# Performance work log

Measured on AMD Instinct MI355X. Metric: run time of the kernel, lower is better.

The kernel has to match this reference:

```python
import jax, jax.numpy as jnp
import numpy as np

NUM_JOINTS = 24
NUM_GRAPHS = 65536
# SMPL-like humanoid kinematic tree: parent[i] < i, root has parent -1
PARENT_TREE = np.array([-1, 0, 1, 2, 3, 0, 5, 6, 7, 0, 9, 10, 11, 12, 11,
                        14, 15, 16, 11, 18, 19, 20, 12, 22], dtype=np.int64)


def rotation_6d_to_matrix(d6):
    # standard 6D rotation representation -> 3x3 rotation matrix (rows b1,b2,b3)
    a1, a2 = d6[..., :3], d6[..., 3:]
    b1 = a1 / (jnp.linalg.norm(a1, axis=-1, keepdims=True) + 1e-12)
    a2p = a2 - jnp.sum(b1 * a2, axis=-1, keepdims=True) * b1
    b2 = a2p / (jnp.linalg.norm(a2p, axis=-1, keepdims=True) + 1e-12)
    b3 = jnp.cross(b1, b2)
    return jnp.stack([b1, b2, b3], axis=-2)  # [..., 3, 3]


def setup_inputs() -> dict:
    key = jax.random.key(0)
    k1, k2 = jax.random.split(key)
    B, N = NUM_GRAPHS, NUM_JOINTS
    x = jax.random.normal(k1, (B * N, 6), dtype=jnp.float32)
    offset = jax.random.normal(k2, (B * N, 3), dtype=jnp.float32)
    parent = jnp.tile(jnp.asarray(PARENT_TREE), B)  # [B*N], valid tree per graph
    return {"x": x, "parent": parent, "offset": offset, "num_graphs": B}


def reference(x, parent, offset, num_graphs):
    B = num_graphs
    x = x.reshape(B, -1, x.shape[-1])            # [B, N, 6]
    N = x.shape[1]
    offset = offset.reshape(B, N, 3)             # [B, N, 3]
    parent_np = np.asarray(parent).reshape(B, -1)[0]  # static tree structure

    T = rotation_6d_to_matrix(x)                 # [B, N, 3, 3] local rotations

    pos = [None] * N   # world positions per joint, each [B, 3]
    rot = [None] * N   # world rotations per joint, each [B, 3, 3]
    for i in range(N):  # N is small/static; parent-before-child order
        p = int(parent_np[i])
        if p == -1:
            pos[i] = jnp.zeros((B, 3), dtype=x.dtype)
            rot[i] = T[:, i]
        else:
            pos[i] = jnp.einsum('bij,bj->bi', rot[p], offset[:, i]) + pos[p]
            rot[i] = jnp.einsum('bij,bjk->bik', rot[p], T[:, i])

    positions = jnp.stack(pos, axis=1)           # [B, N, 3]
    return positions.reshape(-1, 3)              # [B*N, 3]
```

## Files before the change

### kernel.cpp

```cpp
#include <hip/hip_runtime.h>
#include <math.h>


#define GPB 128
#define PAD 129

__device__ __forceinline__ void rot6d(float a0, float a1, float a2,
                                      float a3, float a4, float a5,
                                      float T[9]) {
    float n1 = sqrtf(a0*a0 + a1*a1 + a2*a2) + 1e-12f;
    float i1 = 1.0f / n1;
    float b1x = a0*i1, b1y = a1*i1, b1z = a2*i1;
    float d = b1x*a3 + b1y*a4 + b1z*a5;
    float ax = a3 - d*b1x, ay = a4 - d*b1y, az = a5 - d*b1z;
    float n2 = sqrtf(ax*ax + ay*ay + az*az) + 1e-12f;
    float i2 = 1.0f / n2;
    float b2x = ax*i2, b2y = ay*i2, b2z = az*i2;
    T[0] = b1x; T[1] = b1y; T[2] = b1z;
    T[3] = b2x; T[4] = b2y; T[5] = b2z;
    T[6] = b1y*b2z - b1z*b2y;
    T[7] = b1z*b2x - b1x*b2z;
    T[8] = b1x*b2y - b1y*b2x;
}

__device__ __forceinline__ void load_x(const float4* __restrict__ x4, long base4,
                                       int c, int t, float4 xr[9]) {
#pragma unroll
    for (int k = 0; k < 9; ++k) {
        int i = k * GPB + t;
        int g = i / 9, e = i - g * 9;
        xr[k] = x4[base4 + (long)g * 36 + c * 9 + e];
    }
}

__device__ __forceinline__ void load_o(const float2* __restrict__ o2, long base2,
                                       int c, int t, float2 orr[9]) {
#pragma unroll
    for (int k = 0; k < 9; ++k) {
        int i = k * GPB + t;
        int g = i / 9, e = i - g * 9;
        orr[k] = o2[base2 + (long)g * 36 + c * 9 + e];
    }
}

__device__ __forceinline__ void write_lds(float* xs, float* os_, int t,
                                          const float4 xr[9], const float2 orr[9]) {
#pragma unroll
    for (int k = 0; k < 9; ++k) {
        int i = k * GPB + t;
        int g = i / 9, e = i - g * 9;
        xs[(4*e+0)*PAD + g] = xr[k].x;
        xs[(4*e+1)*PAD + g] = xr[k].y;
        xs[(4*e+2)*PAD + g] = xr[k].z;
        xs[(4*e+3)*PAD + g] = xr[k].w;
        os_[(2*e+0)*PAD + g] = orr[k].x;
        os_[(2*e+1)*PAD + g] = orr[k].y;
    }
}

template<int J>
__device__ __forceinline__ void joint_step(const float* xs, const float* os_,
                                           float* outs, int t,
                                           float R[9], float Pc[3]) {
    constexpr int jl = J % 6;
    float a0 = xs[(jl*6+0)*PAD + t];
    float a1 = xs[(jl*6+1)*PAD + t];
    float a2 = xs[(jl*6+2)*PAD + t];
    float a3 = xs[(jl*6+3)*PAD + t];
    float a4 = xs[(jl*6+4)*PAD + t];
    float a5 = xs[(jl*6+5)*PAD + t];
    float T[9];
    rot6d(a0, a1, a2, a3, a4, a5, T);
    float o0 = os_[(jl*3+0)*PAD + t];
    float o1 = os_[(jl*3+1)*PAD + t];
    float o2 = os_[(jl*3+2)*PAD + t];
    float p0 = R[0]*o0 + R[1]*o1 + R[2]*o2 + Pc[0];
    float p1 = R[3]*o0 + R[4]*o1 + R[5]*o2 + Pc[1];
    float p2 = R[6]*o0 + R[7]*o1 + R[8]*o2 + Pc[2];
    float Rn[9];
#pragma unroll
    for (int i = 0; i < 3; ++i)
#pragma unroll
        for (int k = 0; k < 3; ++k)
            Rn[i*3+k] = R[i*3+0]*T[0+k] + R[i*3+1]*T[3+k] + R[i*3+2]*T[6+k];
#pragma unroll
    for (int i = 0; i < 9; ++i) R[i] = Rn[i];
    Pc[0] = p0; Pc[1] = p1; Pc[2] = p2;
    outs[(J*3+0)*PAD + t] = p0;
    outs[(J*3+1)*PAD + t] = p1;
    outs[(J*3+2)*PAD + t] = p2;
}

__global__ __launch_bounds__(GPB) void fk_kernel(const float* __restrict__ x,
                                                 const float* __restrict__ off,
                                                 float* __restrict__ out, int B) {
    __shared__ float xs[36 * PAD];
    __shared__ float os_[18 * PAD];
    __shared__ float outs[72 * PAD];
    int t = threadIdx.x;
    long gb0 = (long)blockIdx.x * GPB;
    const float4* x4 = (const float4*)x;
    const float2* o2g = (const float2*)off;
    long xb4 = gb0 * 36;
    long ob2 = gb0 * 36;

    float4 xr[9]; float2 orr[9];
    float R[9], Pc[3], R0[9], R11[9], P11[3], R12[9], P12[3];

    load_x(x4, xb4, 0, t, xr);
    load_o(o2g, ob2, 0, t, orr);
    write_lds(xs, os_, t, xr, orr);
    __syncthreads();

    load_x(x4, xb4, 1, t, xr);
    load_o(o2g, ob2, 1, t, orr);
    {
        float a0 = xs[0*PAD+t], a1 = xs[1*PAD+t], a2 = xs[2*PAD+t];
        float a3 = xs[3*PAD+t], a4 = xs[4*PAD+t], a5 = xs[5*PAD+t];
        rot6d(a0, a1, a2, a3, a4, a5, R);
        Pc[0] = Pc[1] = Pc[2] = 0.0f;
        outs[0*PAD+t] = 0.0f; outs[1*PAD+t] = 0.0f; outs[2*PAD+t] = 0.0f;
#pragma unroll
        for (int i = 0; i < 9; ++i) R0[i] = R[i];
    }
    joint_step<1>(xs, os_, outs, t, R, Pc);
    joint_step<2>(xs, os_, outs, t, R, Pc);
    joint_step<3>(xs, os_, outs, t, R, Pc);
    joint_step<4>(xs, os_, outs, t, R, Pc);
#pragma unroll
    for (int i = 0; i < 9; ++i) R[i] = R0[i];
    Pc[0] = Pc[1] = Pc[2] = 0.0f;
    joint_step<5>(xs, os_, outs, t, R, Pc);
    __syncthreads();
    write_lds(xs, os_, t, xr, orr);
    __syncthreads();

    load_x(x4, xb4, 2, t, xr);
    load_o(o2g, ob2, 2, t, orr);
    joint_step<6>(xs, os_, outs, t, R, Pc);
    joint_step<7>(xs, os_, outs, t, R, Pc);
    joint_step<8>(xs, os_, outs, t, R, Pc);
#pragma unroll
    for (int i = 0; i < 9; ++i) R[i] = R0[i];
    Pc[0] = Pc[1] = Pc[2] = 0.0f;
    joint_step<9>(xs, os_, outs, t, R, Pc);
    joint_step<10>(xs, os_, outs, t, R, Pc);
    joint_step<11>(xs, os_, outs, t, R, Pc);
#pragma unroll
    for (int i = 0; i < 9; ++i) R11[i] = R[i];
    P11[0] = Pc[0]; P11[1] = Pc[1]; P11[2] = Pc[2];
    __syncthreads();
    write_lds(xs, os_, t, xr, orr);
    __syncthreads();

    load_x(x4, xb4, 3, t, xr);
    load_o(o2g, ob2, 3, t, orr);
    joint_step<12>(xs, os_, outs, t, R, Pc);
#pragma unroll
    for (int i = 0; i < 9; ++i) R12[i] = R[i];
    P12[0] = Pc[0]; P12[1] = Pc[1]; P12[2] = Pc[2];
    joint_step<13>(xs, os_, outs, t, R, Pc);
#pragma unroll
    for (int i = 0; i < 9; ++i) R[i] = R11[i];
    Pc[0] = P11[0]; Pc[1] = P11[1]; Pc[2] = P11[2];
    joint_step<14>(xs, os_, outs, t, R, Pc);
    joint_step<15>(xs, os_, outs, t, R, Pc);
    joint_step<16>(xs, os_, outs, t, R, Pc);
    joint_step<17>(xs, os_, outs, t, R, Pc);
    __syncthreads();
    write_lds(xs, os_, t, xr, orr);
    __syncthreads();

#pragma unroll
    for (int i = 0; i < 9; ++i) R[i] = R11[i];
    Pc[0] = P11[0]; Pc[1] = P11[1]; Pc[2] = P11[2];
    joint_step<18>(xs, os_, outs, t, R, Pc);
    joint_step<19>(xs, os_, outs, t, R, Pc);
    joint_step<20>(xs, os_, outs, t, R, Pc);
    joint_step<21>(xs, os_, outs, t, R, Pc);
#pragma unroll
    for (int i = 0; i < 9; ++i) R[i] = R12[i];
    Pc[0] = P12[0]; Pc[1] = P12[1]; Pc[2] = P12[2];
    joint_step<22>(xs, os_, outs, t, R, Pc);
    joint_step<23>(xs, os_, outs, t, R, Pc);
    __syncthreads();

    float4* out4 = (float4*)out;
    long outb4 = gb0 * 18;
#pragma unroll
    for (int k = 0; k < 18; ++k) {
        int i = k * GPB + t;
        int g = i / 18, e = i - g * 18;
        float4 v;
        v.x = outs[(4*e+0)*PAD + g];
        v.y = outs[(4*e+1)*PAD + g];
        v.z = outs[(4*e+2)*PAD + g];
        v.w = outs[(4*e+3)*PAD + g];
        out4[outb4 + i] = v;
    }
}

__global__ __launch_bounds__(256) void fk_tail(const float* __restrict__ x,
                                               const float* __restrict__ off,
                                               float* __restrict__ out,
                                               int b0, int B) {
    int b = b0 + blockIdx.x * blockDim.x + threadIdx.x;
    if (b >= B) return;
    const float* xb = x + (size_t)b * 144;
    const float* ob = off + (size_t)b * 72;
    float* P = out + (size_t)b * 72;
    float R[9], Pc[3], R0[9], R11[9], P11[3], R12[9], P12[3];
    {
        rot6d(xb[0], xb[1], xb[2], xb[3], xb[4], xb[5], R);
        Pc[0] = Pc[1] = Pc[2] = 0.0f;
        P[0] = P[1] = P[2] = 0.0f;
        for (int i = 0; i < 9; ++i) R0[i] = R[i];
    }
    const int parent[24] = {-1,0,1,2,3,0,5,6,7,0,9,10,11,12,11,14,15,16,11,18,19,20,12,22};
    for (int j = 1; j < 24; ++j) {
        int p = parent[j];
        float Rp[9], Pp[3];
        if (p == 0)       { for (int i=0;i<9;++i) Rp[i]=R0[i];  Pp[0]=Pp[1]=Pp[2]=0.f; }
        else if (j==14||j==18) { for (int i=0;i<9;++i) Rp[i]=R11[i]; Pp[0]=P11[0];Pp[1]=P11[1];Pp[2]=P11[2]; }
        else if (j==22)   { for (int i=0;i<9;++i) Rp[i]=R12[i]; Pp[0]=P12[0];Pp[1]=P12[1];Pp[2]=P12[2]; }
        else              { for (int i=0;i<9;++i) Rp[i]=R[i];   Pp[0]=Pc[0];Pp[1]=Pc[1];Pp[2]=Pc[2]; }
        float T[9];
        rot6d(xb[j*6+0],xb[j*6+1],xb[j*6+2],xb[j*6+3],xb[j*6+4],xb[j*6+5],T);
        float o0=ob[j*3+0],o1=ob[j*3+1],o2=ob[j*3+2];
        Pc[0]=Rp[0]*o0+Rp[1]*o1+Rp[2]*o2+Pp[0];
        Pc[1]=Rp[3]*o0+Rp[4]*o1+Rp[5]*o2+Pp[1];
        Pc[2]=Rp[6]*o0+Rp[7]*o1+Rp[8]*o2+Pp[2];
        for (int i=0;i<3;++i) for (int k=0;k<3;++k) {
            float s=0.f; for (int m=0;m<3;++m) s+=Rp[i*3+m]*T[m*3+k];
            R[i*3+k]=s;
        }
        P[j*3+0]=Pc[0]; P[j*3+1]=Pc[1]; P[j*3+2]=Pc[2];
        if (j==11) { for (int i=0;i<9;++i) R11[i]=R[i]; P11[0]=Pc[0];P11[1]=Pc[1];P11[2]=Pc[2]; }
        if (j==12) { for (int i=0;i<9;++i) R12[i]=R[i]; P12[0]=Pc[0];P12[1]=Pc[1];P12[2]=Pc[2]; }
    }
}

extern "C" void kernel_launch(void* const* d_in, const int* in_sizes, int n_in,
                              void* d_out, int out_size, void* d_ws, size_t ws_size,
                              hipStream_t stream) {
    const float* x   = (const float*)d_in[0];
    const float* off = (const float*)d_in[2];
    float* out = (float*)d_out;
    int B = in_sizes[0] / 144;
    int nb = B / GPB;
    if (nb > 0)
        fk_kernel<<<nb, GPB, 0, stream>>>(x, off, out, B);
    int rem = B - nb * GPB;
    if (rem > 0)
        fk_tail<<<(rem + 255) / 256, 256, 0, stream>>>(x, off, out, nb * GPB, B);
}
```

Baseline: 22.08 us.

## Prefetch all input chunks up front, halve block size, flush outputs early

Loads all four joint chunks of x and offset into registers at kernel start instead of software-pipelining one chunk ahead, halves graphs per block to 64 so the register arrays fit, and writes the first half of the output positions to global memory mid-kernel. The aim is more memory-level parallelism per thread and overlap of output stores with later compute. Holding 54 vector registers of input per thread sharply raises register pressure and may cut occupancy despite the smaller blocks. Launch bounds now hint one block per CU minimum. The tail kernel also hardcodes the root-child test.

```diff
diff --git a/kernel.cpp b/kernel.cpp
--- a/kernel.cpp
+++ b/kernel.cpp
@@ -2,8 +2,8 @@
 #include <math.h>
 
 
-#define GPB 128
-#define PAD 129
+#define GPB 64
+#define PAD 65
 
 __device__ __forceinline__ void rot6d(float a0, float a1, float a2,
                                       float a3, float a4, float a5,
@@ -21,26 +21,6 @@
     T[6] = b1y*b2z - b1z*b2y;
     T[7] = b1z*b2x - b1x*b2z;
     T[8] = b1x*b2y - b1y*b2x;
-}
-
-__device__ __forceinline__ void load_x(const float4* __restrict__ x4, long base4,
-                                       int c, int t, float4 xr[9]) {
-#pragma unroll
-    for (int k = 0; k < 9; ++k) {
-        int i = k * GPB + t;
-        int g = i / 9, e = i - g * 9;
-        xr[k] = x4[base4 + (long)g * 36 + c * 9 + e];
-    }
-}
-
-__device__ __forceinline__ void load_o(const float2* __restrict__ o2, long base2,
-                                       int c, int t, float2 orr[9]) {
-#pragma unroll
-    for (int k = 0; k < 9; ++k) {
-        int i = k * GPB + t;
-        int g = i / 9, e = i - g * 9;
-        orr[k] = o2[base2 + (long)g * 36 + c * 9 + e];
-    }
 }
 
 __device__ __forceinline__ void write_lds(float* xs, float* os_, int t,
@@ -91,9 +71,25 @@
     outs[(J*3+2)*PAD + t] = p2;
 }
 
-__global__ __launch_bounds__(GPB) void fk_kernel(const float* __restrict__ x,
-                                                 const float* __restrict__ off,
-                                                 float* __restrict__ out, int B) {
+template<int H>
+__device__ __forceinline__ void flush_half(const float* outs, float4* out4,
+                                           long outb4, int t) {
+#pragma unroll
+    for (int k = 0; k < 9; ++k) {
+        int i = k * GPB + t;
+        int g = i / 9, e = i - g * 9;
+        float4 v;
+        v.x = outs[(36*H + 4*e + 0)*PAD + g];
+        v.y = outs[(36*H + 4*e + 1)*PAD + g];
+        v.z = outs[(36*H + 4*e + 2)*PAD + g];
+        v.w = outs[(36*H + 4*e + 3)*PAD + g];
+        out4[outb4 + (long)g*18 + 9*H + e] = v;
+    }
+}
+
+__global__ __launch_bounds__(GPB, 1) void fk_kernel(const float* __restrict__ x,
+                                                    const float* __restrict__ off,
+                                                    float* __restrict__ out, int B) {
     __shared__ float xs[36 * PAD];
     __shared__ float os_[18 * PAD];
     __shared__ float outs[72 * PAD];
@@ -104,16 +100,30 @@
     long xb4 = gb0 * 36;
     long ob2 = gb0 * 36;
 
-    float4 xr[9]; float2 orr[9];
+    float4 xr[4][9];
+    float2 orr[4][9];
+#pragma unroll
+    for (int c = 0; c < 4; ++c) {
+#pragma unroll
+        for (int k = 0; k < 9; ++k) {
+            int i = k * GPB + t;
+            int g = i / 9, e = i - g * 9;
+            xr[c][k] = x4[xb4 + (long)g * 36 + c * 9 + e];
+        }
+#pragma unroll
+        for (int k = 0; k < 9; ++k) {
+            int i = k * GPB + t;
+            int g = i / 9, e = i - g * 9;
+            orr[c][k] = o2g[ob2 + (long)g * 36 + c * 9 + e];
+        }
+    }
+
     float R[9], Pc[3], R0[9], R11[9], P11[3], R12[9], P12[3];
-
-    load_x(x4, xb4, 0, t, xr);
-    load_o(o2g, ob2, 0, t, orr);
-    write_lds(xs, os_, t, xr, orr);
-    __syncthreads();
-
-    load_x(x4, xb4, 1, t, xr);
-    load_o(o2g, ob2, 1, t, orr);
+    float4* out4 = (float4*)out;
+    long outb4 = gb0 * 18;
+
+    write_lds(xs, os_, t, xr[0], orr[0]);
+    __syncthreads();
     {
         float a0 = xs[0*PAD+t], a1 = xs[1*PAD+t], a2 = xs[2*PAD+t];
         float a3 = xs[3*PAD+t], a4 = xs[4*PAD+t], a5 = xs[5*PAD+t];
@@ -132,11 +142,9 @@
     Pc[0] = Pc[1] = Pc[2] = 0.0f;
     joint_step<5>(xs, os_, outs, t, R, Pc);
     __syncthreads();
-    write_lds(xs, os_, t, xr, orr);
-    __syncthreads();
-
-    load_x(x4, xb4, 2, t, xr);
-    load_o(o2g, ob2, 2, t, orr);
+
+    write_lds(xs, os_, t, xr[1], orr[1]);
+    __syncthreads();
     joint_step<6>(xs, os_, outs, t, R, Pc);
     joint_step<7>(xs, os_, outs, t, R, Pc);
     joint_step<8>(xs, os_, outs, t, R, Pc);
@@ -149,12 +157,11 @@
 #pragma unroll
     for (int i = 0; i < 9; ++i) R11[i] = R[i];
     P11[0] = Pc[0]; P11[1] = Pc[1]; P11[2] = Pc[2];
-    __syncthreads();
-    write_lds(xs, os_, t, xr, orr);
-    __syncthreads();
-
-    load_x(x4, xb4, 3, t, xr);
-    load_o(o2g, ob2, 3, t, orr);
+    flush_half<0>(outs, out4, outb4, t);
+    __syncthreads();
+
+    write_lds(xs, os_, t, xr[2], orr[2]);
+    __syncthreads();
     joint_step<12>(xs, os_, outs, t, R, Pc);
 #pragma unroll
     for (int i = 0; i < 9; ++i) R12[i] = R[i];
@@ -168,9 +175,9 @@
     joint_step<16>(xs, os_, outs, t, R, Pc);
     joint_step<17>(xs, os_, outs, t, R, Pc);
     __syncthreads();
-    write_lds(xs, os_, t, xr, orr);
-    __syncthreads();
-
+
+    write_lds(xs, os_, t, xr[3], orr[3]);
+    __syncthreads();
 #pragma unroll
     for (int i = 0; i < 9; ++i) R[i] = R11[i];
     Pc[0] = P11[0]; Pc[1] = P11[1]; Pc[2] = P11[2];
@@ -183,21 +190,7 @@
     Pc[0] = P12[0]; Pc[1] = P12[1]; Pc[2] = P12[2];
     joint_step<22>(xs, os_, outs, t, R, Pc);
     joint_step<23>(xs, os_, outs, t, R, Pc);
-    __syncthreads();
-
-    float4* out4 = (float4*)out;
-    long outb4 = gb0 * 18;
-#pragma unroll
-    for (int k = 0; k < 18; ++k) {
-        int i = k * GPB + t;
-        int g = i / 18, e = i - g * 18;
-        float4 v;
-        v.x = outs[(4*e+0)*PAD + g];
-        v.y = outs[(4*e+1)*PAD + g];
-        v.z = outs[(4*e+2)*PAD + g];
-        v.w = outs[(4*e+3)*PAD + g];
-        out4[outb4 + i] = v;
-    }
+    flush_half<1>(outs, out4, outb4, t);
 }
 
 __global__ __launch_bounds__(256) void fk_tail(const float* __restrict__ x,
@@ -216,11 +209,9 @@
         P[0] = P[1] = P[2] = 0.0f;
         for (int i = 0; i < 9; ++i) R0[i] = R[i];
     }
-    const int parent[24] = {-1,0,1,2,3,0,5,6,7,0,9,10,11,12,11,14,15,16,11,18,19,20,12,22};
     for (int j = 1; j < 24; ++j) {
-        int p = parent[j];
         float Rp[9], Pp[3];
-        if (p == 0)       { for (int i=0;i<9;++i) Rp[i]=R0[i];  Pp[0]=Pp[1]=Pp[2]=0.f; }
+        if (j==1||j==5||j==9) { for (int i=0;i<9;++i) Rp[i]=R0[i]; Pp[0]=Pp[1]=Pp[2]=0.f; }
         else if (j==14||j==18) { for (int i=0;i<9;++i) Rp[i]=R11[i]; Pp[0]=P11[0];Pp[1]=P11[1];Pp[2]=P11[2]; }
         else if (j==22)   { for (int i=0;i<9;++i) Rp[i]=R12[i]; Pp[0]=P12[0];Pp[1]=P12[1];Pp[2]=P12[2]; }
         else              { for (int i=0;i<9;++i) Rp[i]=R[i];   Pp[0]=Pc[0];Pp[1]=Pc[1];Pp[2]=Pc[2]; }
```

After: 24.44 us. +10.7%, slower.
